# Optimization experiments

Hardware: AMD Instinct MI355X
Metric: run time of the kernel (lower is better)

## Reference

```python
import jax, jax.numpy as jnp
import numpy as np

B, S, DIM, NH = 256, 64, 1024, 8
DH = DIM // NH
EPS = 1e-6
LN_EPS = 1e-5


def _make_hops(n):
    hops = np.zeros((n, n), dtype=np.int64)
    cur = 1
    for i in range(n):
        for j in range(i + 1, n):
            hops[i, j] = cur
            hops[j, i] = cur
            cur += 1
    return hops, cur


def setup_inputs() -> dict:
    key = jax.random.key(0)
    ks = jax.random.split(key, 8)
    hops_np, curnum = _make_hops(S)
    return {
        "q": jax.random.normal(ks[0], (B, S, DIM), dtype=jnp.float32),
        "k": jax.random.normal(ks[1], (B, S, DIM), dtype=jnp.float32),
        "v": jax.random.normal(ks[2], (B, S, DIM), dtype=jnp.float32),
        "igate_w": jax.random.normal(ks[3], (NH, 3 * DIM), dtype=jnp.float32) * 0.02,
        "igate_b": jax.random.normal(ks[4], (NH,), dtype=jnp.float32) * 0.1,
        "fgate_w": jax.random.normal(ks[5], (NH, 3 * DIM), dtype=jnp.float32) * 0.02,
        "fgate_b": jnp.linspace(3.0, 6.0, NH, dtype=jnp.float32),
        "rpe": jax.random.normal(ks[6], (curnum, DIM), dtype=jnp.float32) * 0.02,
        "ln_w": jax.random.normal(ks[7], (DIM,), dtype=jnp.float32) * 0.1,
        "ln_b": jnp.zeros((DIM,), dtype=jnp.float32),
        "hops": jnp.asarray(hops_np),
    }


def _mlstm_forward(q, k, v, igate_w, igate_b, fgate_w, fgate_b, rpe, ln_w, ln_b, hops):
    Bq, Sq, _ = q.shape
    pos_emb = rpe[hops]                                   # (S, S, DIM)
    gate_in = jnp.concatenate([q, k, v], axis=-1)         # (B, S, 3*DIM)
    ig = gate_in @ igate_w.T + igate_b                    # (B, S, NH)
    fg = gate_in @ fgate_w.T + fgate_b                    # (B, S, NH)
    ig = jnp.transpose(ig, (0, 2, 1))                     # (B, NH, S)
    fg = jnp.transpose(fg, (0, 2, 1))                     # (B, NH, S)

    qh = q.reshape(Bq, Sq, NH, DH).transpose(0, 2, 1, 3)  # (B, NH, S, DH)
    kh = k.reshape(Bq, Sq, NH, DH).transpose(0, 2, 1, 3)
    vh = v.reshape(Bq, Sq, NH, DH).transpose(0, 2, 1, 3)

    # log forget gates, cumulative sum with a leading zero
    log_f = jax.nn.log_sigmoid(fg)                        # (B, NH, S)
    csum = jnp.cumsum(log_f, axis=-1)
    csum = jnp.concatenate([jnp.zeros((Bq, NH, 1), csum.dtype), csum], axis=-1)  # (B,NH,S+1)
    lfm = csum[:, :, :, None] - csum[:, :, None, :]       # (B, NH, S+1, S+1)
    ltr = jnp.tril(jnp.ones((Sq, Sq), dtype=bool))
    log_fg_matrix = jnp.where(ltr, lfm[:, :, 1:, 1:], -jnp.inf)  # (B, NH, S, S)

    log_D = log_fg_matrix + ig[:, :, None, :]             # add i-gate per column
    max_log_D = jnp.max(log_D, axis=-1, keepdims=True)    # rowwise stabilization
    D = jnp.exp(log_D - max_log_D)                        # (B, NH, S, S)

    k_scaled = kh / np.sqrt(DH).astype(np.float32)
    pe = pos_emb.reshape(Sq, Sq, NH, DH)
    k_hop = jnp.einsum('bhvc,vmhc->bhvm', qh, pe)         # (B, NH, S, S)
    qk = jnp.einsum('bhsd,bhtd->bhst', qh, k_scaled)      # (B, NH, S, S)
    C = (qk + k_hop) * D

    normalizer = jnp.maximum(jnp.abs(jnp.sum(C, axis=-1, keepdims=True)), jnp.exp(-max_log_D))
    Cn = C / (normalizer + EPS)
    h = Cn @ vh                                           # (B, NH, S, DH)

    # MultiHeadLayerNorm == group_norm with NH groups: normalize each head over DH
    mu = jnp.mean(h, axis=-1, keepdims=True)
    var = jnp.mean(jnp.square(h - mu), axis=-1, keepdims=True)
    hn = (h - mu) / jnp.sqrt(var + LN_EPS)
    w = (1.0 + ln_w).reshape(NH, DH)                      # residual weight: 1 + w
    b = ln_b.reshape(NH, DH)
    hn = hn * w[None, :, None, :] + b[None, :, None, :]
    return hn.transpose(0, 2, 1, 3).reshape(Bq, Sq, DIM)


def reference(q, k, v, igate_w, igate_b, fgate_w, fgate_b, rpe, ln_w, ln_b, hops):
    return _mlstm_forward(q, k, v, igate_w, igate_b, fgate_w, fgate_b, rpe, ln_w, ln_b, hops)
```

## Files before the change

### kernel.cpp

```cpp
#include <hip/hip_runtime.h>
#include <math.h>

#define BB 256
#define SS 64
#define DIMM 1024
#define NHH 8
#define DHH 128

typedef short bf16x8 __attribute__((ext_vector_type(8)));
typedef float f32x4 __attribute__((ext_vector_type(4)));

__device__ __forceinline__ unsigned cvtpk(float lo, float hi) {
    unsigned r;
    asm("v_cvt_pk_bf16_f32 %0, %1, %2" : "=v"(r) : "v"(lo), "v"(hi));
    return r;
}
__device__ __forceinline__ unsigned pk2(float lo, float hi) { return cvtpk(lo, hi); }
__device__ __forceinline__ unsigned short f2bh(float x) {
    return (unsigned short)(cvtpk(x, 0.0f) & 0xFFFFu);
}
__device__ __forceinline__ float bf2f(unsigned short b) {
    union { unsigned u; float f; } x{((unsigned)b) << 16};
    return x.f;
}
__device__ __forceinline__ void split2(float a, float b, unsigned& hi, unsigned& lo) {
    hi = cvtpk(a, b);
    const float ha = __uint_as_float(hi << 16);
    const float hb = __uint_as_float(hi & 0xFFFF0000u);
    lo = cvtpk(a - ha, b - hb);
}
__device__ __forceinline__ float logsigf(float x) {
    return fminf(x, 0.0f) - log1pf(__expf(-fabsf(x)));
}

__global__ __launch_bounds__(256) void k_gate_mfma(
    const float* __restrict__ q, const float* __restrict__ k, const float* __restrict__ v,
    const float* __restrict__ igw, const float* __restrict__ fgw,
    float* __restrict__ part)
{
    __shared__ unsigned short Xs[64 * 264];
    __shared__ unsigned short Ws[16 * 264];
    const int b = blockIdx.x & 255;
    const int ksl = blockIdx.x >> 8;
    const int t = threadIdx.x;
    const int w = t >> 6, l = t & 63, c = l & 15, g = l >> 4;

    f32x4 acc;
    acc[0] = 0.f; acc[1] = 0.f; acc[2] = 0.f; acc[3] = 0.f;

    for (int step = 0; step < 3; ++step) {
        const int kc = ksl * 3 + step;
        const int tensor = kc >> 2;
        const float* src = (tensor == 0) ? q : (tensor == 1) ? k : v;
        src += (size_t)b * 65536 + (kc & 3) * 256;

        float4 xb[16];
        #pragma unroll
        for (int i = 0; i < 16; ++i)
            xb[i] = *reinterpret_cast<const float4*>(src + (size_t)(4 * i + w) * 1024 + 4 * l);
        const int o = t >> 4, wseg = t & 15;
        const float* wp = (o < 8 ? igw + o * 3072 : fgw + (o - 8) * 3072)
                          + ksl * 768 + step * 256;
        float4 wb4[4];
        #pragma unroll
        for (int e = 0; e < 4; ++e)
            wb4[e] = *reinterpret_cast<const float4*>(wp + e * 64 + wseg * 4);

        #pragma unroll
        for (int i = 0; i < 16; ++i) {
            unsigned* dp = reinterpret_cast<unsigned*>(&Xs[(4 * i + w) * 264 + 4 * l]);
            dp[0] = pk2(xb[i].x, xb[i].y); dp[1] = pk2(xb[i].z, xb[i].w);
        }
        #pragma unroll
        for (int e = 0; e < 4; ++e) {
            unsigned* dp = reinterpret_cast<unsigned*>(&Ws[o * 264 + e * 64 + wseg * 4]);
            dp[0] = pk2(wb4[e].x, wb4[e].y); dp[1] = pk2(wb4[e].z, wb4[e].w);
        }
        __syncthreads();
        #pragma unroll
        for (int kk = 0; kk < 8; ++kk) {
            bf16x8 a  = *reinterpret_cast<const bf16x8*>(&Xs[(16 * w + c) * 264 + 32 * kk + 8 * g]);
            bf16x8 bw = *reinterpret_cast<const bf16x8*>(&Ws[c * 264 + 32 * kk + 8 * g]);
            acc = __builtin_amdgcn_mfma_f32_16x16x32_bf16(a, bw, acc, 0, 0, 0);
        }
        __syncthreads();
    }
    float* pb = part + (((size_t)ksl * 256 + b) * 64) * 16;
    #pragma unroll
    for (int reg = 0; reg < 4; ++reg) {
        const int s = 16 * w + 4 * g + reg;
        pb[s * 16 + c] = acc[reg];
    }
}

__global__ __launch_bounds__(256) void k_gates_final(
    const float* __restrict__ part, const float* __restrict__ igb, const float* __restrict__ fgb,
    float* __restrict__ ig_ws, float* __restrict__ csum_ws, float* __restrict__ pmax_ws)
{
    const int b = blockIdx.x;
    const int t = threadIdx.x;
    __shared__ float red[64][18];
    {
        const int s = t >> 2, oq = t & 3;
        float4 sum = make_float4(0.f, 0.f, 0.f, 0.f);
        #pragma unroll
        for (int ksl = 0; ksl < 4; ++ksl) {
            const float4 p = *reinterpret_cast<const float4*>(
                part + (((size_t)ksl * 256 + b) * 64 + s) * 16 + oq * 4);
            sum.x += p.x; sum.y += p.y; sum.z += p.z; sum.w += p.w;
        }
        red[s][oq * 4 + 0] = sum.x; red[s][oq * 4 + 1] = sum.y;
        red[s][oq * 4 + 2] = sum.z; red[s][oq * 4 + 3] = sum.w;
    }
    __syncthreads();
    if (t < 64) {
        const int s = t;
        #pragma unroll
        for (int h = 0; h < 8; ++h) {
            float ig = red[s][h]     + igb[h];
            float fg = red[s][8 + h] + fgb[h];
            float lf = logsigf(fg);
            float cs = lf;
            #pragma unroll
            for (int d = 1; d < 64; d <<= 1) {
                float o = __shfl_up(cs, (unsigned)d, 64);
                if (s >= d) cs += o;
            }
            float pm = ig - cs;
            #pragma unroll
            for (int d = 1; d < 64; d <<= 1) {
                float o = __shfl_up(pm, (unsigned)d, 64);
                if (s >= d) pm = fmaxf(pm, o);
            }
            const int base = b * NHH + h;
            ig_ws[base * SS + s] = ig;
            csum_ws[base * 65 + s + 1] = cs;
            if (s == 0) csum_ws[base * 65] = 0.0f;
            pmax_ws[base * SS + s] = pm;
        }
    }
}

__global__ __launch_bounds__(256) void k_khop(
    const float* __restrict__ q, const float* __restrict__ rpe, const int* __restrict__ hops,
    float* __restrict__ khop_ws)
{
    __shared__ unsigned short Phi[64 * 136];
    __shared__ unsigned short Plo[64 * 136];
    const int v = blockIdx.x;
    const int h = blockIdx.y;
    const int t = threadIdx.x;
    const int w = t >> 6, l = t & 63, c = l & 15, g = l >> 4;

    const int npair = (v + 1) * 64;
    unsigned* PhiU = reinterpret_cast<unsigned*>(Phi);
    unsigned* PloU = reinterpret_cast<unsigned*>(Plo);
    for (int idx = t; idx < npair; idx += 256) {
        const int m = idx >> 6, cp = idx & 63;
        const float2 x = *reinterpret_cast<const float2*>(
            rpe + (size_t)hops[v * SS + m] * DIMM + h * DHH + 2 * cp);
        unsigned hi, lo;
        split2(x.x, x.y, hi, lo);
        PhiU[m * 68 + cp] = hi;
        PloU[m * 68 + cp] = lo;
    }
    __syncthreads();

    const int ntiles = (v >> 4) + 1;
    union bfu { unsigned u[4]; bf16x8 vv; };
    #pragma unroll
    for (int ms = 0; ms < 4; ++ms) {
        const int brow = 64 * w + 16 * ms + c;
        const float* qbase = q + ((size_t)brow * SS + v) * DIMM + h * DHH + 8 * g;
        bfu qhi[4], qlo[4];
        #pragma unroll
        for (int kk = 0; kk < 4; ++kk) {
            const float4 f0 = *reinterpret_cast<const float4*>(qbase + 32 * kk);
            const float4 f1 = *reinterpret_cast<const float4*>(qbase + 32 * kk + 4);
            split2(f0.x, f0.y, qhi[kk].u[0], qlo[kk].u[0]);
            split2(f0.z, f0.w, qhi[kk].u[1], qlo[kk].u[1]);
            split2(f1.x, f1.y, qhi[kk].u[2], qlo[kk].u[2]);
            split2(f1.z, f1.w, qhi[kk].u[3], qlo[kk].u[3]);
        }
        for (int n = 0; n < ntiles; ++n) {
            f32x4 acc;
            acc[0] = 0.f; acc[1] = 0.f; acc[2] = 0.f; acc[3] = 0.f;
            #pragma unroll
            for (int kk = 0; kk < 4; ++kk) {
                const int off = (16 * n + c) * 136 + 32 * kk + 8 * g;
                bf16x8 bhi = *reinterpret_cast<const bf16x8*>(&Phi[off]);
                bf16x8 blo = *reinterpret_cast<const bf16x8*>(&Plo[off]);
                acc = __builtin_amdgcn_mfma_f32_16x16x32_bf16(qhi[kk].vv, bhi, acc, 0, 0, 0);
                acc = __builtin_amdgcn_mfma_f32_16x16x32_bf16(qlo[kk].vv, bhi, acc, 0, 0, 0);
                acc = __builtin_amdgcn_mfma_f32_16x16x32_bf16(qhi[kk].vv, blo, acc, 0, 0, 0);
            }
            #pragma unroll
            for (int reg = 0; reg < 4; ++reg) {
                const int bo = 64 * w + 16 * ms + 4 * g + reg;
                khop_ws[(((size_t)bo * NHH + h) * SS + v) * SS + 16 * n + c] = acc[reg];
            }
        }
    }
}

__global__ __launch_bounds__(256) void k_attn(
    const float* __restrict__ q, const float* __restrict__ k, const float* __restrict__ v,
    const float* __restrict__ lnw, const float* __restrict__ lnb,
    const float* __restrict__ ig_ws, const float* __restrict__ csum_ws,
    const float* __restrict__ pmax_ws, const float* __restrict__ khop_ws,
    float* __restrict__ out)
{
    __shared__ __attribute__((aligned(16))) unsigned short Kspl[2 * 64 * 136];
    __shared__ float csum_s[65];
    __shared__ float ig_s[64];
    __shared__ float pmax_s[64];
    __shared__ float lnw_s[128];
    __shared__ float lnb_s[128];

    const int bid = blockIdx.x;
    const int b = bid >> 3, h = bid & 7;
    const int t = threadIdx.x;
    const int w = t >> 6, l = t & 63, c = l & 15, g = l >> 4;
    const float rs_dh = 0.08838834764831845f;

    unsigned short* Khi = Kspl;
    unsigned short* Klo = Kspl + 64 * 136;

    float4 vreg[2][4];
    #pragma unroll
    for (int it = 0; it < 2; ++it) {
        const int u = t + 256 * it;
        const int jp = u >> 4, seg8 = u & 15;
        const float* r0 = v + ((size_t)(b * 64 + 2 * jp)) * 1024 + h * 128 + seg8 * 8;
        vreg[it][0] = *reinterpret_cast<const float4*>(r0);
        vreg[it][1] = *reinterpret_cast<const float4*>(r0 + 4);
        vreg[it][2] = *reinterpret_cast<const float4*>(r0 + 1024);
        vreg[it][3] = *reinterpret_cast<const float4*>(r0 + 1028);
    }

    float kh[4][4];
    {
        const float* khb = khop_ws + ((size_t)(b * NHH + h) * SS) * SS;
        #pragma unroll
        for (int n = 0; n < 4; ++n) {
            if (n > w) continue;
            #pragma unroll
            for (int reg = 0; reg < 4; ++reg) {
                const int i = 16 * w + 4 * g + reg;
                kh[n][reg] = khb[(size_t)i * SS + 16 * n + c];
            }
        }
    }

    #pragma unroll
    for (int it = 0; it < 2; ++it) {
        const int u = t + 256 * it;
        const int row = u >> 3, seg = u & 7;
        const float* kp = k + ((size_t)(b * 64 + row)) * 1024 + h * 128;
        #pragma unroll
        for (int e = 0; e < 2; ++e) {
            const int col = e * 64 + seg * 8;
            const float4 ya = *reinterpret_cast<const float4*>(kp + col);
            const float4 yb = *reinterpret_cast<const float4*>(kp + col + 4);
            unsigned* dh = reinterpret_cast<unsigned*>(&Khi[row * 136 + col]);
            unsigned* dl = reinterpret_cast<unsigned*>(&Klo[row * 136 + col]);
            split2(ya.x * rs_dh, ya.y * rs_dh, dh[0], dl[0]);
            split2(ya.z * rs_dh, ya.w * rs_dh, dh[1], dl[1]);
            split2(yb.x * rs_dh, yb.y * rs_dh, dh[2], dl[2]);
            split2(yb.z * rs_dh, yb.w * rs_dh, dh[3], dl[3]);
        }
    }
    const int cb = b * NHH + h;
    if (t < 65) csum_s[t] = csum_ws[cb * 65 + t];
    if (t >= 128 && t < 192) ig_s[t - 128] = ig_ws[cb * SS + (t - 128)];
    if (t >= 192) pmax_s[t - 192] = pmax_ws[cb * SS + (t - 192)];
    if (t < 128) lnw_s[t] = lnw[h * 128 + t];
    else if (t < 256) lnb_s[t - 128] = lnb[h * 128 + (t - 128)];

    union bfu { unsigned u[4]; bf16x8 v; };
    bfu qhi[4], qlo[4];
    {
        const int qrow = 16 * w + c;
        const float* qbase = q + ((size_t)(b * 64 + qrow)) * 1024 + h * 128 + 8 * g;
        #pragma unroll
        for (int kk = 0; kk < 4; ++kk) {
            const float4 f0 = *reinterpret_cast<const float4*>(qbase + 32 * kk);
            const float4 f1 = *reinterpret_cast<const float4*>(qbase + 32 * kk + 4);
            split2(f0.x, f0.y, qhi[kk].u[0], qlo[kk].u[0]);
            split2(f0.z, f0.w, qhi[kk].u[1], qlo[kk].u[1]);
            split2(f1.x, f1.y, qhi[kk].u[2], qlo[kk].u[2]);
            split2(f1.z, f1.w, qhi[kk].u[3], qlo[kk].u[3]);
        }
    }
    __syncthreads();

    f32x4 acc[4];
    #pragma unroll
    for (int n = 0; n < 4; ++n) { acc[n][0]=0.f; acc[n][1]=0.f; acc[n][2]=0.f; acc[n][3]=0.f; }
    #pragma unroll
    for (int kk = 0; kk < 4; ++kk) {
        #pragma unroll
        for (int n = 0; n < 4; ++n) {
            if (n > w) continue;
            const int off = (16 * n + c) * 136 + 32 * kk + 8 * g;
            bf16x8 bhi = *reinterpret_cast<const bf16x8*>(&Khi[off]);
            bf16x8 blo = *reinterpret_cast<const bf16x8*>(&Klo[off]);
            acc[n] = __builtin_amdgcn_mfma_f32_16x16x32_bf16(qhi[kk].v, bhi, acc[n], 0, 0, 0);
            acc[n] = __builtin_amdgcn_mfma_f32_16x16x32_bf16(qlo[kk].v, bhi, acc[n], 0, 0, 0);
            acc[n] = __builtin_amdgcn_mfma_f32_16x16x32_bf16(qhi[kk].v, blo, acc[n], 0, 0, 0);
        }
    }
    __syncthreads();

    unsigned short* VT = Kspl;
    unsigned short* Cn = Kspl + 128 * 72;
    #pragma unroll
    for (int it = 0; it < 2; ++it) {
        const int u = t + 256 * it;
        const int jp = u >> 4, seg8 = u & 15;
        float v0[8], v1[8];
        v0[0]=vreg[it][0].x; v0[1]=vreg[it][0].y; v0[2]=vreg[it][0].z; v0[3]=vreg[it][0].w;
        v0[4]=vreg[it][1].x; v0[5]=vreg[it][1].y; v0[6]=vreg[it][1].z; v0[7]=vreg[it][1].w;
        v1[0]=vreg[it][2].x; v1[1]=vreg[it][2].y; v1[2]=vreg[it][2].z; v1[3]=vreg[it][2].w;
        v1[4]=vreg[it][3].x; v1[5]=vreg[it][3].y; v1[6]=vreg[it][3].z; v1[7]=vreg[it][3].w;
        #pragma unroll
        for (int m = 0; m < 8; ++m) {
            const int cc = seg8 * 8 + m;
            unsigned byte = (unsigned)(cc * 144 + 4 * jp);
            byte ^= ((cc >> 3) & 7) << 4;
            *reinterpret_cast<unsigned*>(reinterpret_cast<char*>(VT) + byte) = pk2(v0[m], v1[m]);
        }
    }

    {
        float mi[4], rs[4];
        #pragma unroll
        for (int reg = 0; reg < 4; ++reg) {
            const int i = 16 * w + 4 * g + reg;
            mi[reg] = csum_s[i + 1] + pmax_s[i];
            rs[reg] = 0.0f;
        }
        #pragma unroll
        for (int n = 0; n < 4; ++n) {
            if (n > w) continue;
            const int j = 16 * n + c;
            const float cj = csum_s[j + 1], igj = ig_s[j];
            #pragma unroll
            for (int reg = 0; reg < 4; ++reg) {
                const int i = 16 * w + 4 * g + reg;
                float val = 0.0f;
                if (j <= i) {
                    const float sc = acc[n][reg] + kh[n][reg];
                    val = sc * __expf(csum_s[i + 1] - cj + igj - mi[reg]);
                }
                acc[n][reg] = val;
                rs[reg] += val;
            }
        }
        #pragma unroll
        for (int reg = 0; reg < 4; ++reg) {
            float r = rs[reg];
            r += __shfl_xor(r, 1); r += __shfl_xor(r, 2);
            r += __shfl_xor(r, 4); r += __shfl_xor(r, 8);
            const float nrm = fmaxf(fabsf(r), __expf(-mi[reg]));
            const float inv = 1.0f / (nrm + 1e-6f);
            const int i = 16 * w + 4 * g + reg;
            #pragma unroll
            for (int n = 0; n < 4; ++n) {
                const int j = 16 * n + c;
                Cn[i * 72 + j] = f2bh(acc[n][reg] * inv);
            }
        }
    }
    __syncthreads();

    f32x4 hacc[8];
    #pragma unroll
    for (int n = 0; n < 8; ++n) { hacc[n][0]=0.f; hacc[n][1]=0.f; hacc[n][2]=0.f; hacc[n][3]=0.f; }
    #pragma unroll
    for (int ks = 0; ks < 2; ++ks) {
        bf16x8 a = *reinterpret_cast<const bf16x8*>(&Cn[(16 * w + c) * 72 + 32 * ks + 8 * g]);
        #pragma unroll
        for (int n = 0; n < 8; ++n) {
            const int cc = 16 * n + c;
            unsigned byte = (unsigned)(cc * 144 + 64 * ks + 16 * g);
            byte ^= ((cc >> 3) & 7) << 4;
            bf16x8 bv = *reinterpret_cast<const bf16x8*>(reinterpret_cast<const char*>(VT) + byte);
            hacc[n] = __builtin_amdgcn_mfma_f32_16x16x32_bf16(a, bv, hacc[n], 0, 0, 0);
        }
    }

    #pragma unroll
    for (int reg = 0; reg < 4; ++reg) {
        float s1 = 0.f, s2 = 0.f;
        #pragma unroll
        for (int n = 0; n < 8; ++n) { const float x = hacc[n][reg]; s1 += x; s2 = fmaf(x, x, s2); }
        s1 += __shfl_xor(s1, 1); s1 += __shfl_xor(s1, 2);
        s1 += __shfl_xor(s1, 4); s1 += __shfl_xor(s1, 8);
        s2 += __shfl_xor(s2, 1); s2 += __shfl_xor(s2, 2);
        s2 += __shfl_xor(s2, 4); s2 += __shfl_xor(s2, 8);
        const float mu = s1 * (1.0f / 128.0f);
        const float var = s2 * (1.0f / 128.0f) - mu * mu;
        const float rstd = rsqrtf(var + 1e-5f);
        const int io = 16 * w + 4 * g + reg;
        float* op = out + (((size_t)(b * 64 + io)) * 8 + h) * 128;
        #pragma unroll
        for (int n = 0; n < 8; ++n) {
            const int cc = 16 * n + c;
            op[cc] = (hacc[n][reg] - mu) * rstd * (1.0f + lnw_s[cc]) + lnb_s[cc];
        }
    }
}

extern "C" void kernel_launch(void* const* d_in, const int* in_sizes, int n_in,
                              void* d_out, int out_size, void* d_ws, size_t ws_size,
                              hipStream_t stream) {
    const float* q   = (const float*)d_in[0];
    const float* k   = (const float*)d_in[1];
    const float* v   = (const float*)d_in[2];
    const float* igw = (const float*)d_in[3];
    const float* igb = (const float*)d_in[4];
    const float* fgw = (const float*)d_in[5];
    const float* fgb = (const float*)d_in[6];
    const float* rpe = (const float*)d_in[7];
    const float* lnw = (const float*)d_in[8];
    const float* lnb = (const float*)d_in[9];
    const int*  hops = (const int*)d_in[10];
    float* out = (float*)d_out;

    float* ig_ws   = (float*)d_ws;
    float* pmax_ws = ig_ws + 131072;
    float* csum_ws = pmax_ws + 131072;
    float* part    = csum_ws + 133120;
    float* khop_ws = part;

    hipLaunchKernelGGL(k_gate_mfma, dim3(1024), dim3(256), 0, stream,
                       q, k, v, igw, fgw, part);
    hipLaunchKernelGGL(k_gates_final, dim3(BB), dim3(256), 0, stream,
                       part, igb, fgb, ig_ws, csum_ws, pmax_ws);
    hipLaunchKernelGGL(k_khop, dim3(SS, NHH), dim3(256), 0, stream,
                       q, rpe, hops, khop_ws);
    hipLaunchKernelGGL(k_attn, dim3(BB * NHH), dim3(256), 0, stream,
                       q, k, v, lnw, lnb, ig_ws, csum_ws, pmax_ws, khop_ws, out);
}
```

Measured before the change: 128.9 us.

## Merge gate projection and k_hop kernels into one launch with separate workspaces

The gate-projection GEMM and the k_hop positional-term kernel become one horizontally fused kernel. Block IDs below 512 compute k_hop and the rest compute gate partials, with shared memory sized for the larger of the two bodies. This needs separate workspace regions for the gate partials and k_hop instead of aliasing them, so the new path runs only when the workspace is large enough and otherwise falls back to the old four-launch sequence. The aim is to drop one launch and let the two independent stages fill the GPU together, at the cost of higher shared memory per block for the k_hop blocks.

```diff
diff --git a/kernel.cpp b/kernel.cpp
--- a/kernel.cpp
+++ b/kernel.cpp
@@ -33,18 +33,13 @@
     return fminf(x, 0.0f) - log1pf(__expf(-fabsf(x)));
 }
 
-__global__ __launch_bounds__(256) void k_gate_mfma(
+__device__ __forceinline__ void gate_body(
+    int b, int ksl, int t,
     const float* __restrict__ q, const float* __restrict__ k, const float* __restrict__ v,
     const float* __restrict__ igw, const float* __restrict__ fgw,
-    float* __restrict__ part)
-{
-    __shared__ unsigned short Xs[64 * 264];
-    __shared__ unsigned short Ws[16 * 264];
-    const int b = blockIdx.x & 255;
-    const int ksl = blockIdx.x >> 8;
-    const int t = threadIdx.x;
+    float* __restrict__ part, unsigned short* Xs, unsigned short* Ws)
+{
     const int w = t >> 6, l = t & 63, c = l & 15, g = l >> 4;
-
     f32x4 acc;
     acc[0] = 0.f; acc[1] = 0.f; acc[2] = 0.f; acc[3] = 0.f;
 
@@ -93,72 +88,19 @@
     }
 }
 
-__global__ __launch_bounds__(256) void k_gates_final(
-    const float* __restrict__ part, const float* __restrict__ igb, const float* __restrict__ fgb,
-    float* __restrict__ ig_ws, float* __restrict__ csum_ws, float* __restrict__ pmax_ws)
-{
-    const int b = blockIdx.x;
-    const int t = threadIdx.x;
-    __shared__ float red[64][18];
-    {
-        const int s = t >> 2, oq = t & 3;
-        float4 sum = make_float4(0.f, 0.f, 0.f, 0.f);
-        #pragma unroll
-        for (int ksl = 0; ksl < 4; ++ksl) {
-            const float4 p = *reinterpret_cast<const float4*>(
-                part + (((size_t)ksl * 256 + b) * 64 + s) * 16 + oq * 4);
-            sum.x += p.x; sum.y += p.y; sum.z += p.z; sum.w += p.w;
-        }
-        red[s][oq * 4 + 0] = sum.x; red[s][oq * 4 + 1] = sum.y;
-        red[s][oq * 4 + 2] = sum.z; red[s][oq * 4 + 3] = sum.w;
-    }
-    __syncthreads();
-    if (t < 64) {
-        const int s = t;
-        #pragma unroll
-        for (int h = 0; h < 8; ++h) {
-            float ig = red[s][h]     + igb[h];
-            float fg = red[s][8 + h] + fgb[h];
-            float lf = logsigf(fg);
-            float cs = lf;
-            #pragma unroll
-            for (int d = 1; d < 64; d <<= 1) {
-                float o = __shfl_up(cs, (unsigned)d, 64);
-                if (s >= d) cs += o;
-            }
-            float pm = ig - cs;
-            #pragma unroll
-            for (int d = 1; d < 64; d <<= 1) {
-                float o = __shfl_up(pm, (unsigned)d, 64);
-                if (s >= d) pm = fmaxf(pm, o);
-            }
-            const int base = b * NHH + h;
-            ig_ws[base * SS + s] = ig;
-            csum_ws[base * 65 + s + 1] = cs;
-            if (s == 0) csum_ws[base * 65] = 0.0f;
-            pmax_ws[base * SS + s] = pm;
-        }
-    }
-}
-
-__global__ __launch_bounds__(256) void k_khop(
+__device__ __forceinline__ void khop_body(
+    int vb, int h, int t,
     const float* __restrict__ q, const float* __restrict__ rpe, const int* __restrict__ hops,
-    float* __restrict__ khop_ws)
-{
-    __shared__ unsigned short Phi[64 * 136];
-    __shared__ unsigned short Plo[64 * 136];
-    const int v = blockIdx.x;
-    const int h = blockIdx.y;
-    const int t = threadIdx.x;
+    float* __restrict__ khop_ws, unsigned short* Phi, unsigned short* Plo)
+{
     const int w = t >> 6, l = t & 63, c = l & 15, g = l >> 4;
-
-    const int npair = (v + 1) * 64;
+    const int npair = (vb + 1) * 64;
     unsigned* PhiU = reinterpret_cast<unsigned*>(Phi);
     unsigned* PloU = reinterpret_cast<unsigned*>(Plo);
     for (int idx = t; idx < npair; idx += 256) {
         const int m = idx >> 6, cp = idx & 63;
         const float2 x = *reinterpret_cast<const float2*>(
-            rpe + (size_t)hops[v * SS + m] * DIMM + h * DHH + 2 * cp);
+            rpe + (size_t)hops[vb * SS + m] * DIMM + h * DHH + 2 * cp);
         unsigned hi, lo;
         split2(x.x, x.y, hi, lo);
         PhiU[m * 68 + cp] = hi;
@@ -166,12 +108,12 @@
     }
     __syncthreads();
 
-    const int ntiles = (v >> 4) + 1;
+    const int ntiles = (vb >> 4) + 1;
     union bfu { unsigned u[4]; bf16x8 vv; };
     #pragma unroll
     for (int ms = 0; ms < 4; ++ms) {
         const int brow = 64 * w + 16 * ms + c;
-        const float* qbase = q + ((size_t)brow * SS + v) * DIMM + h * DHH + 8 * g;
+        const float* qbase = q + ((size_t)brow * SS + vb) * DIMM + h * DHH + 8 * g;
         bfu qhi[4], qlo[4];
         #pragma unroll
         for (int kk = 0; kk < 4; ++kk) {
@@ -197,8 +139,94 @@
             #pragma unroll
             for (int reg = 0; reg < 4; ++reg) {
                 const int bo = 64 * w + 16 * ms + 4 * g + reg;
-                khop_ws[(((size_t)bo * NHH + h) * SS + v) * SS + 16 * n + c] = acc[reg];
-            }
+                khop_ws[(((size_t)bo * NHH + h) * SS + vb) * SS + 16 * n + c] = acc[reg];
+            }
+        }
+    }
+}
+
+__global__ __launch_bounds__(256) void k_gate_khop(
+    const float* __restrict__ q, const float* __restrict__ k, const float* __restrict__ v,
+    const float* __restrict__ igw, const float* __restrict__ fgw,
+    const float* __restrict__ rpe, const int* __restrict__ hops,
+    float* __restrict__ part, float* __restrict__ khop_ws)
+{
+    __shared__ __attribute__((aligned(16))) char smem[80 * 264 * 2];
+    const int bid = blockIdx.x;
+    const int t = threadIdx.x;
+    if (bid < 512) {
+        unsigned short* Phi = reinterpret_cast<unsigned short*>(smem);
+        khop_body(bid & 63, bid >> 6, t, q, rpe, hops, khop_ws, Phi, Phi + 64 * 136);
+    } else {
+        const int gb = bid - 512;
+        unsigned short* Xs = reinterpret_cast<unsigned short*>(smem);
+        gate_body(gb & 255, gb >> 8, t, q, k, v, igw, fgw, part, Xs, Xs + 64 * 264);
+    }
+}
+
+__global__ __launch_bounds__(256) void k_gate_mfma(
+    const float* __restrict__ q, const float* __restrict__ k, const float* __restrict__ v,
+    const float* __restrict__ igw, const float* __restrict__ fgw,
+    float* __restrict__ part)
+{
+    __shared__ unsigned short Xs[64 * 264];
+    __shared__ unsigned short Ws[16 * 264];
+    gate_body(blockIdx.x & 255, blockIdx.x >> 8, threadIdx.x, q, k, v, igw, fgw, part, Xs, Ws);
+}
+
+__global__ __launch_bounds__(256) void k_khop(
+    const float* __restrict__ q, const float* __restrict__ rpe, const int* __restrict__ hops,
+    float* __restrict__ khop_ws)
+{
+    __shared__ unsigned short Phi[64 * 136];
+    __shared__ unsigned short Plo[64 * 136];
+    khop_body(blockIdx.x, blockIdx.y, threadIdx.x, q, rpe, hops, khop_ws, Phi, Plo);
+}
+
+__global__ __launch_bounds__(256) void k_gates_final(
+    const float* __restrict__ part, const float* __restrict__ igb, const float* __restrict__ fgb,
+    float* __restrict__ ig_ws, float* __restrict__ csum_ws, float* __restrict__ pmax_ws)
+{
+    const int b = blockIdx.x;
+    const int t = threadIdx.x;
+    __shared__ float red[64][18];
+    {
+        const int s = t >> 2, oq = t & 3;
+        float4 sum = make_float4(0.f, 0.f, 0.f, 0.f);
+        #pragma unroll
+        for (int ksl = 0; ksl < 4; ++ksl) {
+            const float4 p = *reinterpret_cast<const float4*>(
+                part + (((size_t)ksl * 256 + b) * 64 + s) * 16 + oq * 4);
+            sum.x += p.x; sum.y += p.y; sum.z += p.z; sum.w += p.w;
+        }
+        red[s][oq * 4 + 0] = sum.x; red[s][oq * 4 + 1] = sum.y;
+        red[s][oq * 4 + 2] = sum.z; red[s][oq * 4 + 3] = sum.w;
+    }
+    __syncthreads();
+    if (t < 64) {
+        const int s = t;
+        #pragma unroll
+        for (int h = 0; h < 8; ++h) {
+            float ig = red[s][h]     + igb[h];
+            float fg = red[s][8 + h] + fgb[h];
+            float lf = logsigf(fg);
+            float cs = lf;
+            #pragma unroll
+            for (int d = 1; d < 64; d <<= 1) {
+                float o = __shfl_up(cs, (unsigned)d, 64);
+                if (s >= d) cs += o;
+            }
+            float pm = ig - cs;
+            #pragma unroll
+            for (int d = 1; d < 64; d <<= 1) {
+                float o = __shfl_up(pm, (unsigned)d, 64);
+                if (s >= d) pm = fmaxf(pm, o);
+            }
+            const int base = b * NHH + h;
+            ig_ws[base * SS + s] = ig;
+            csum_ws[base * 65 + s + 1] = cs;
+            if (s == 0) csum_ws[base * 65] = 0.0f;
+            pmax_ws[base * SS + s] = pm;
         }
     }
 }
@@ -432,14 +460,25 @@
     float* pmax_ws = ig_ws + 131072;
     float* csum_ws = pmax_ws + 131072;
     float* part    = csum_ws + 133120;
-    float* khop_ws = part;
-
-    hipLaunchKernelGGL(k_gate_mfma, dim3(1024), dim3(256), 0, stream,
-                       q, k, v, igw, fgw, part);
-    hipLaunchKernelGGL(k_gates_final, dim3(BB), dim3(256), 0, stream,
-                       part, igb, fgb, ig_ws, csum_ws, pmax_ws);
-    hipLaunchKernelGGL(k_khop, dim3(SS, NHH), dim3(256), 0, stream,
-                       q, rpe, hops, khop_ws);
-    hipLaunchKernelGGL(k_attn, dim3(BB * NHH), dim3(256), 0, stream,
-                       q, k, v, lnw, lnb, ig_ws, csum_ws, pmax_ws, khop_ws, out);
-}
+
+    const size_t NEED = (size_t)(131072 + 131072 + 133120 + 1048576 + 8388608) * 4;
+    if (ws_size >= NEED) {
+        float* khop_ws = part + 1048576;
+        hipLaunchKernelGGL(k_gate_khop, dim3(1536), dim3(256), 0, stream,
+                           q, k, v, igw, fgw, rpe, hops, part, khop_ws);
+        hipLaunchKernelGGL(k_gates_final, dim3(BB), dim3(256), 0, stream,
+                           part, igb, fgb, ig_ws, csum_ws, pmax_ws);
+        hipLaunchKernelGGL(k_attn, dim3(BB * NHH), dim3(256), 0, stream,
+                           q, k, v, lnw, lnb, ig_ws, csum_ws, pmax_ws, khop_ws, out);
+    } else {
+        float* khop_ws = part;
+        hipLaunchKernelGGL(k_gate_mfma, dim3(1024), dim3(256), 0, stream,
+                           q, k, v, igw, fgw, part);
+        hipLaunchKernelGGL(k_gates_final, dim3(BB), dim3(256), 0, stream,
+                           part, igb, fgb, ig_ws, csum_ws, pmax_ws);
+        hipLaunchKernelGGL(k_khop, dim3(SS, NHH), dim3(256), 0, stream,
+                           q, rpe, hops, khop_ws);
+        hipLaunchKernelGGL(k_attn, dim3(BB * NHH), dim3(256), 0, stream,
+                           q, k, v, lnw, lnb, ig_ws, csum_ws, pmax_ws, khop_ws, out);
+    }
+}
```

After: 118.7 us. 1.09x faster.
